# Kernel optimization log

Measured on AMD Instinct MI355X. Metric: run time of the kernel, lower is better.

Reference implementation:

```python
import jax, jax.numpy as jnp
import numpy as np
import math

D_MODEL = 1024
N_HEADS = 16
D_K = D_MODEL // N_HEADS
ROPE_BASE = 10000.0


def rope_cos_sin(seq_len, d_k, base=ROPE_BASE, dtype=jnp.float32):
    inv_freq = 1.0 / base ** (jnp.arange(0, d_k, 2, dtype=dtype) / d_k)  # [d_k/2]
    pos = jnp.arange(seq_len, dtype=dtype)
    freqs = jnp.outer(pos, inv_freq)  # [T, d_k/2]
    return jnp.cos(freqs), jnp.sin(freqs)


def apply_rope(x, cos, sin):
    # x: [B, H, T, d_k]; cos/sin: [T, d_k/2]
    x1 = x[..., 0::2]
    x2 = x[..., 1::2]
    c = cos[None, None]
    s = sin[None, None]
    r1 = x1 * c - x2 * s
    r2 = x1 * s + x2 * c
    return jnp.stack([r1, r2], axis=-1).reshape(x.shape)


def setup_inputs() -> dict:
    key = jax.random.key(0)
    ks = jax.random.split(key, 7)
    B, T = 2, 2048
    scale = 1.0 / math.sqrt(D_MODEL)
    return {
        "query": jax.random.normal(ks[0], (B, T, D_MODEL), jnp.float32),
        "key": jax.random.normal(ks[1], (B, T, D_MODEL), jnp.float32),
        "value": jax.random.normal(ks[2], (B, T, D_MODEL), jnp.float32),
        "Wq": jax.random.normal(ks[3], (D_MODEL, D_MODEL), jnp.float32) * scale,
        "Wk": jax.random.normal(ks[4], (D_MODEL, D_MODEL), jnp.float32) * scale,
        "Wv": jax.random.normal(ks[5], (D_MODEL, D_MODEL), jnp.float32) * scale,
        "Wo": jax.random.normal(ks[6], (D_MODEL, D_MODEL), jnp.float32) * scale,
    }


def reference(query, key, value, Wq, Wk, Wv, Wo):
    B, Tq, _ = query.shape
    Tk = key.shape[1]
    # nn.Linear: x @ W.T
    Q = (query @ Wq.T).reshape(B, Tq, N_HEADS, D_K).transpose(0, 2, 1, 3)
    K = (key @ Wk.T).reshape(B, Tk, N_HEADS, D_K).transpose(0, 2, 1, 3)
    V = (value @ Wv.T).reshape(B, Tk, N_HEADS, D_K).transpose(0, 2, 1, 3)
    cos_q, sin_q = rope_cos_sin(Tq, D_K)
    cos_k, sin_k = rope_cos_sin(Tk, D_K)
    Q = apply_rope(Q, cos_q, sin_q)
    K = apply_rope(K, cos_k, sin_k)
    scores = jnp.einsum("bhqd,bhkd->bhqk", Q, K) / math.sqrt(D_K)
    attn = jax.nn.softmax(scores, axis=-1)
    out = jnp.einsum("bhqk,bhkd->bhqd", attn, V)
    out = out.transpose(0, 2, 1, 3).reshape(B, Tq, D_MODEL)
    return out @ Wo.T
```

## Files before the change

kernel.cpp:

```cpp
#include <hip/hip_runtime.h>
#include <hip/hip_bf16.h>
#include <cstdint>

typedef unsigned short u16;
typedef __attribute__((ext_vector_type(4))) float fl4;
typedef __attribute__((ext_vector_type(2))) float fl2;
typedef __attribute__((ext_vector_type(4))) unsigned short u16x4;
typedef __attribute__((ext_vector_type(8))) unsigned short u16x8;
typedef __attribute__((ext_vector_type(2))) unsigned int u32x2;
typedef __attribute__((ext_vector_type(8))) __bf16 bf16x8;
typedef __attribute__((ext_vector_type(4))) float f32x4;

#define MKE 4194304
#define NKE 1048576

static __device__ __forceinline__ u16 f2bf(float x) {
  unsigned int u = __builtin_bit_cast(unsigned int, x);
  u += 0x7fffu + ((u >> 16) & 1u);
  return (u16)(u >> 16);
}

static __device__ __forceinline__ unsigned int cvtpk(float a, float b) {
  unsigned int r;
  asm("v_cvt_pk_bf16_f32 %0, %1, %2" : "=v"(r) : "v"(a), "v"(b));
  return r;
}

static __device__ __forceinline__ f32x4 mfma16(bf16x8 a, bf16x8 b, f32x4 c) {
  return __builtin_amdgcn_mfma_f32_16x16x32_bf16(a, b, c, 0, 0, 0);
}

static __device__ __forceinline__ void gload_lds16(const void* g, void* l) {
  __builtin_amdgcn_global_load_lds((const __attribute__((address_space(1))) void*)g,
                                   (__attribute__((address_space(3))) void*)l,
                                   16, 0, 0);
}

__global__ __launch_bounds__(256) void k_prep(const float* __restrict__ q,
                                              const float* __restrict__ k,
                                              const float* __restrict__ v,
                                              const float* __restrict__ wq,
                                              const float* __restrict__ wk,
                                              const float* __restrict__ wv,
                                              const float* __restrict__ wo,
                                              u16* __restrict__ ws,
                                              float* __restrict__ tab) {
  const int bid = blockIdx.x;
  if (bid >= 16384) {
    const int idx = (bid - 16384) * 256 + threadIdx.x;
    const int t = idx >> 5, i = idx & 31;
    const float ang = (float)t * exp2f(-0.4152410118609203f * (float)i);
    float sn, cs;
    sincosf(ang, &sn, &cs);
    reinterpret_cast<fl2*>(tab)[idx] = (fl2){cs, sn};
    return;
  }
  const int i = bid * 256 + threadIdx.x;
  const float* src;
  u16* dst;
  int loc;
  if (i < 3 * 1048576) {
    const int seg = i >> 20;
    loc = i & 1048575;
    src = seg == 0 ? q : (seg == 1 ? k : v);
    dst = ws + (size_t)seg * MKE;
  } else {
    const int j = i - 3 * 1048576;
    const int seg = j >> 18;
    loc = j & 262143;
    src = seg == 0 ? wq : (seg == 1 ? wk : (seg == 2 ? wv : wo));
    dst = ws + 3 * (size_t)MKE + (size_t)seg * NKE;
  }
  fl4 val = reinterpret_cast<const fl4*>(src)[loc];
  u16x4 o;
  o[0] = f2bf(val[0]); o[1] = f2bf(val[1]); o[2] = f2bf(val[2]); o[3] = f2bf(val[3]);
  reinterpret_cast<u16x4*>(dst)[loc] = o;
}

__global__ __launch_bounds__(256) void k_gemm_qkv(
    const u16* __restrict__ aq, const u16* __restrict__ ak, const u16* __restrict__ av,
    const u16* __restrict__ bq, const u16* __restrict__ bk, const u16* __restrict__ bv,
    u16* __restrict__ cq, u16* __restrict__ ck, u16* __restrict__ cv,
    const fl2* __restrict__ tab) {
  constexpr int K = 1024;
  __shared__ __align__(16) u16 smem[16384];
  u16* sA = smem;
  u16* sB = smem + 8192;
  const int z = blockIdx.z;
  const u16* A  = z == 0 ? aq : (z == 1 ? ak : av);
  const u16* Bw = z == 0 ? bq : (z == 1 ? bk : bv);
  u16* C        = z == 0 ? cq : (z == 1 ? ck : cv);
  const float scale = (z == 0) ? 0.18033688011112042f : 1.0f;

  const int tid = threadIdx.x;
  const int w = tid >> 6, lane = tid & 63;
  const int wm = w >> 1, wn = w & 1;
  const int trow = blockIdx.y << 7, tcol = blockIdx.x << 7;
  const int l15 = lane & 15, l4 = lane >> 4;
  const int srow = lane >> 3;
  const int scol = ((lane & 7) ^ srow) << 3;

  f32x4 acc[4][4];
#pragma unroll
  for (int m = 0; m < 4; ++m)
#pragma unroll
    for (int n = 0; n < 4; ++n) acc[m][n] = (f32x4){0.f, 0.f, 0.f, 0.f};

  for (int k0 = 0; k0 < K; k0 += 64) {
#pragma unroll
    for (int c = 0; c < 4; ++c) {
      const int g = c * 4 + w;
      const int row = g * 8 + srow;
      gload_lds16(A + (size_t)(trow + row) * K + (k0 + scol), (void*)(sA + g * 512));
      gload_lds16(Bw + (size_t)(tcol + row) * K + (k0 + scol), (void*)(sB + g * 512));
    }
    __syncthreads();
#pragma unroll
    for (int kc = 0; kc < 2; ++kc) {
      const int kb = (kc * 32 + l4 * 8) * 2;
      bf16x8 af[4], bfr[4];
#pragma unroll
      for (int m = 0; m < 4; ++m) {
        const int r = wm * 64 + m * 16 + l15;
        af[m] = *reinterpret_cast<const bf16x8*>(
            reinterpret_cast<const char*>(sA) + r * 128 + (kb ^ ((r & 7) << 4)));
      }
#pragma unroll
      for (int n = 0; n < 4; ++n) {
        const int r = wn * 64 + n * 16 + l15;
        bfr[n] = *reinterpret_cast<const bf16x8*>(
            reinterpret_cast<const char*>(sB) + r * 128 + (kb ^ ((r & 7) << 4)));
      }
      __builtin_amdgcn_s_setprio(1);
#pragma unroll
      for (int m = 0; m < 4; ++m)
#pragma unroll
        for (int n = 0; n < 4; ++n)
          acc[m][n] = mfma16(af[m], bfr[n], acc[m][n]);
      __builtin_amdgcn_s_setprio(0);
    }
    __syncthreads();
  }

  if (z < 2) {
#pragma unroll
    for (int m = 0; m < 4; ++m) {
#pragma unroll
      for (int n = 0; n < 4; ++n) {
#pragma unroll
        for (int r = 0; r < 4; ++r) {
          const float vsc = acc[m][n][r] * scale;
          const int row = trow + wm * 64 + m * 16 + l4 * 4 + r;
          const int col = tcol + wn * 64 + n * 16 + l15;
          const int b = row >> 11, t = row & 2047;
          const int h = col >> 6, d = col & 63;
          const float partner = __shfl_xor(vsc, 1);
          const fl2 cs = tab[t * 32 + (d >> 1)];
          const float outv =
              (d & 1) ? (partner * cs.y + vsc * cs.x) : (vsc * cs.x - partner * cs.y);
          C[((size_t)((b << 4) + h) * 2048 + t) * 64 + d] = f2bf(outv);
        }
      }
    }
  } else {
#pragma unroll
    for (int m = 0; m < 4; ++m)
#pragma unroll
      for (int n = 0; n < 4; ++n)
#pragma unroll
        for (int r = 0; r < 4; ++r) {
          const int c = wn * 64 + n * 16 + l15;
          const int rl = wm * 64 + m * 16 + l4 * 4 + r;
          smem[c * 128 + (rl ^ ((c & 15) * 8))] = f2bf(acc[m][n][r]);
        }
    __syncthreads();
    const int bq = trow >> 11;
    const int tb = trow & 2047;
#pragma unroll
    for (int j = 0; j < 8; ++j) {
      const int flat = (tid + j * 256) * 8;
      const int c = flat >> 7, r0 = flat & 127;
      u16x8 vv = *reinterpret_cast<const u16x8*>(smem + c * 128 + (r0 ^ ((c & 15) * 8)));
      const int col = tcol + c;
      u16* dst = C + ((size_t)((bq << 4) + (col >> 6)) * 64 + (col & 63)) * 2048 + tb + r0;
      *reinterpret_cast<u16x8*>(dst) = vv;
    }
  }
}

__global__ __launch_bounds__(256) void k_gemm_o(const u16* __restrict__ A,
                                                const u16* __restrict__ Bw,
                                                float* __restrict__ C) {
  constexpr int K = 1024, N = 1024;
  __shared__ __align__(16) u16 sA[2][128 * 64];
  __shared__ __align__(16) u16 sB[2][64 * 64];
  const int tid = threadIdx.x;
  const int w = tid >> 6, lane = tid & 63;
  const int wm = w >> 1, wn = w & 1;
  const int trow = blockIdx.y << 7, tcol = blockIdx.x << 6;
  const int l15 = lane & 15, l4 = lane >> 4;
  const int srow = lane >> 3;
  const int scol = ((lane & 7) ^ srow) << 3;

  f32x4 acc[4][2];
#pragma unroll
  for (int m = 0; m < 4; ++m)
#pragma unroll
    for (int n = 0; n < 2; ++n) acc[m][n] = (f32x4){0.f, 0.f, 0.f, 0.f};

  auto stage = [&](int k0, int buf) {
#pragma unroll
    for (int c = 0; c < 4; ++c) {
      const int g = c * 4 + w;
      const int row = g * 8 + srow;
      gload_lds16(A + (size_t)(trow + row) * K + (k0 + scol), (void*)(sA[buf] + g * 512));
    }
#pragma unroll
    for (int c = 0; c < 2; ++c) {
      const int g = c * 4 + w;
      const int row = g * 8 + srow;
      gload_lds16(Bw + (size_t)(tcol + row) * K + (k0 + scol), (void*)(sB[buf] + g * 512));
    }
  };

  stage(0, 0);
  __syncthreads();

  for (int t = 0; t < 16; ++t) {
    const int buf = t & 1;
    if (t + 1 < 16) stage((t + 1) * 64, buf ^ 1);
#pragma unroll
    for (int kc = 0; kc < 2; ++kc) {
      const int kb = (kc * 32 + l4 * 8) * 2;
      bf16x8 af[4], bfr[2];
#pragma unroll
      for (int m = 0; m < 4; ++m) {
        const int r = wm * 64 + m * 16 + l15;
        af[m] = *reinterpret_cast<const bf16x8*>(
            reinterpret_cast<const char*>(sA[buf]) + r * 128 + (kb ^ ((r & 7) << 4)));
      }
#pragma unroll
      for (int n = 0; n < 2; ++n) {
        const int r = wn * 32 + n * 16 + l15;
        bfr[n] = *reinterpret_cast<const bf16x8*>(
            reinterpret_cast<const char*>(sB[buf]) + r * 128 + (kb ^ ((r & 7) << 4)));
      }
      __builtin_amdgcn_s_setprio(1);
#pragma unroll
      for (int m = 0; m < 4; ++m)
#pragma unroll
        for (int n = 0; n < 2; ++n)
          acc[m][n] = mfma16(af[m], bfr[n], acc[m][n]);
      __builtin_amdgcn_s_setprio(0);
    }
    __syncthreads();
  }

#pragma unroll
  for (int m = 0; m < 4; ++m)
#pragma unroll
    for (int n = 0; n < 2; ++n)
#pragma unroll
      for (int r = 0; r < 4; ++r) {
        const int row = trow + wm * 64 + m * 16 + l4 * 4 + r;
        const int col = tcol + wn * 32 + n * 16 + l15;
        C[(size_t)row * N + col] = acc[m][n][r];
      }
}

__global__ __launch_bounds__(256) void k_attn(const u16* __restrict__ Q,
                                              const u16* __restrict__ Kh,
                                              const u16* __restrict__ Vt,
                                              u16* __restrict__ Oout) {
  __shared__ __align__(16) char lds[81920];
  const int tid = threadIdx.x;
  const int w = tid >> 6, lane = tid & 63;
  const int l15 = lane & 15, l4 = lane >> 4;
  const int nb = blockIdx.x;
  const int xcd = nb & 7, idx = nb >> 3;
  const int bh = xcd * 4 + (idx >> 4);
  const int q0 = (idx & 15) << 7;

  const u16* Qg = Q + (size_t)bh * (2048 * 64);
  const u16* Kg = Kh + (size_t)bh * (2048 * 64);
  const u16* Vg = Vt + (size_t)bh * (64 * 2048);

  const int swz = (l15 & 7) << 4;
  const int rk0 = l15 * 128 + ((l4 * 16) ^ swz);
  const int rk1 = rk0 ^ 64;
  const int pbase = 65536 + w * 4096 + l15 * 128;
  int pwvA[4];
#pragma unroll
  for (int nn = 0; nn < 4; ++nn) pwvA[nn] = pbase + (((nn * 32) | (l4 * 8)) ^ swz);
  const int rpA0 = pbase + ((l4 * 16) ^ swz);
  const int rpA1 = rpA0 ^ 64;
  const int wst = w * 1024;

  const int srow8 = lane >> 3;
  const int scol = ((lane & 7) ^ srow8) << 3;
  const u16* gK = Kg + (size_t)(w * 8 + srow8) * 64 + scol;
  const u16* gV = Vg + (size_t)(w * 8 + srow8) * 2048 + scol;

  bf16x8 qf0, qf1, qf2, qf3;
  {
    const u16* qpA = Qg + (size_t)(q0 + w * 32 + l15) * 64 + l4 * 8;
    qf0 = *reinterpret_cast<const bf16x8*>(qpA);
    qf1 = *reinterpret_cast<const bf16x8*>(qpA + 32);
    const u16* qpB = qpA + 16 * 64;
    qf2 = *reinterpret_cast<const bf16x8*>(qpB);
    qf3 = *reinterpret_cast<const bf16x8*>(qpB + 32);
  }

  f32x4 oA[4], oB[4];
#pragma unroll
  for (int nn = 0; nn < 4; ++nn) {
    oA[nn] = (f32x4){0.f, 0.f, 0.f, 0.f};
    oB[nn] = (f32x4){0.f, 0.f, 0.f, 0.f};
  }
  float lrunA = 0.f, lrunB = 0.f;

#define STAGE(BUF, STEP)                                                         \
  {                                                                              \
    const int ke = (STEP) * 8192;                                                \
    gload_lds16(gK + ke,        lds + (BUF) + wst);                              \
    gload_lds16(gK + ke + 2048, lds + (BUF) + wst + 4096);                       \
    gload_lds16(gK + ke + 4096, lds + (BUF) + wst + 8192);                       \
    gload_lds16(gK + ke + 6144, lds + (BUF) + wst + 12288);                      \
    const int ve = (STEP) * 128;                                                 \
    gload_lds16(gV + ve,             lds + 32768 + (BUF) + wst);                 \
    gload_lds16(gV + ve + 65536,     lds + 32768 + (BUF) + wst + 4096);          \
    gload_lds16(gV + ve + 64,        lds + 32768 + (BUF) + wst + 8192);          \
    gload_lds16(gV + ve + 65536 + 64, lds + 32768 + (BUF) + wst + 12288);        \
  }

#define ATTN_BODY(KOFF, VOFF)                                                    \
  {                                                                              \
    f32x4 sA[4], sB[4];                                                          \
    __builtin_amdgcn_s_setprio(1);                                               \
    _Pragma("unroll")                                                            \
    for (int nn = 0; nn < 4; ++nn) {                                             \
      bf16x8 kf = *(const bf16x8*)(lds + (KOFF) + rk0 + nn * 2048);              \
      sA[nn] = mfma16(kf, qf0, (f32x4){0.f, 0.f, 0.f, 0.f});                     \
      sB[nn] = mfma16(kf, qf2, (f32x4){0.f, 0.f, 0.f, 0.f});                     \
    }                                                                            \
    _Pragma("unroll")                                                            \
    for (int nn = 0; nn < 4; ++nn) {                                             \
      bf16x8 kf = *(const bf16x8*)(lds + (KOFF) + rk1 + nn * 2048);              \
      sA[nn] = mfma16(kf, qf1, sA[nn]);                                          \
      sB[nn] = mfma16(kf, qf3, sB[nn]);                                          \
    }                                                                            \
    __builtin_amdgcn_s_setprio(0);                                               \
    float ppA[4][4], ppB[4][4];                                                  \
    _Pragma("unroll")                                                            \
    for (int nn = 0; nn < 4; ++nn) {                                             \
      ppA[nn][0] = __builtin_amdgcn_exp2f(sA[nn][0]);                            \
      ppA[nn][1] = __builtin_amdgcn_exp2f(sA[nn][1]);                            \
      ppA[nn][2] = __builtin_amdgcn_exp2f(sA[nn][2]);                            \
      ppA[nn][3] = __builtin_amdgcn_exp2f(sA[nn][3]);                            \
      ppB[nn][0] = __builtin_amdgcn_exp2f(sB[nn][0]);                            \
      ppB[nn][1] = __builtin_amdgcn_exp2f(sB[nn][1]);                            \
      ppB[nn][2] = __builtin_amdgcn_exp2f(sB[nn][2]);                            \
      ppB[nn][3] = __builtin_amdgcn_exp2f(sB[nn][3]);                            \
    }                                                                            \
    _Pragma("unroll")                                                            \
    for (int nn = 0; nn < 4; ++nn) {                                             \
      u32x2 pkA, pkB;                                                            \
      pkA[0] = cvtpk(ppA[nn][0], ppA[nn][1]);                                    \
      pkA[1] = cvtpk(ppA[nn][2], ppA[nn][3]);                                    \
      pkB[0] = cvtpk(ppB[nn][0], ppB[nn][1]);                                    \
      pkB[1] = cvtpk(ppB[nn][2], ppB[nn][3]);                                    \
      *(u32x2*)(lds + pwvA[nn]) = pkA;                                           \
      *(u32x2*)(lds + pwvA[nn] + 2048) = pkB;                                    \
    }                                                                            \
    float rsA = ((ppA[0][0] + ppA[0][1]) + (ppA[0][2] + ppA[0][3])) +            \
                ((ppA[1][0] + ppA[1][1]) + (ppA[1][2] + ppA[1][3])) +            \
                ((ppA[2][0] + ppA[2][1]) + (ppA[2][2] + ppA[2][3])) +            \
                ((ppA[3][0] + ppA[3][1]) + (ppA[3][2] + ppA[3][3]));             \
    float rsB = ((ppB[0][0] + ppB[0][1]) + (ppB[0][2] + ppB[0][3])) +            \
                ((ppB[1][0] + ppB[1][1]) + (ppB[1][2] + ppB[1][3])) +            \
                ((ppB[2][0] + ppB[2][1]) + (ppB[2][2] + ppB[2][3])) +            \
                ((ppB[3][0] + ppB[3][1]) + (ppB[3][2] + ppB[3][3]));             \
    rsA += __shfl_xor(rsA, 16);                                                  \
    rsA += __shfl_xor(rsA, 32);                                                  \
    rsB += __shfl_xor(rsB, 16);                                                  \
    rsB += __shfl_xor(rsB, 32);                                                  \
    lrunA += rsA;                                                                \
    lrunB += rsB;                                                                \
    __builtin_amdgcn_s_setprio(1);                                               \
    _Pragma("unroll")                                                            \
    for (int kc = 0; kc < 2; ++kc) {                                             \
      const bf16x8 pfA = *(const bf16x8*)(lds + (kc ? rpA1 : rpA0));             \
      const bf16x8 pfB = *(const bf16x8*)(lds + (kc ? rpA1 : rpA0) + 2048);      \
      const int rkk = kc ? rk1 : rk0;                                            \
      _Pragma("unroll")                                                          \
      for (int nn = 0; nn < 4; ++nn) {                                           \
        bf16x8 vf = *(const bf16x8*)(lds + (VOFF) + rkk + nn * 2048);            \
        oA[nn] = mfma16(pfA, vf, oA[nn]);                                        \
        oB[nn] = mfma16(pfB, vf, oB[nn]);                                        \
      }                                                                          \
    }                                                                            \
    __builtin_amdgcn_s_setprio(0);                                               \
  }

  STAGE(0, 0)
  __syncthreads();

  int cur = 0;
  for (int c = 0; c < 16; ++c) {
    if (c < 15) STAGE(cur ^ 16384, c + 1)
    ATTN_BODY(cur, 32768 + cur)
    ATTN_BODY(cur + 8192, 32768 + cur + 8192)
    __syncthreads();
    cur ^= 16384;
  }
#undef ATTN_BODY
#undef STAGE

  const int b = bh >> 4, h = bh & 15;
  float lrA[4], lrB[4];
#pragma unroll
  for (int r = 0; r < 4; ++r) {
    const int src = (lane & 48) | (l4 * 4 + r);
    lrA[r] = 1.f / __shfl(lrunA, src);
    lrB[r] = 1.f / __shfl(lrunB, src);
  }
#pragma unroll
  for (int nn = 0; nn < 4; ++nn)
#pragma unroll
    for (int r = 0; r < 4; ++r) {
      const int tA = q0 + w * 32 + l4 * 4 + r;
      const int d = nn * 16 + l15;
      Oout[((size_t)(b * 2048 + tA)) * 1024 + h * 64 + d] = f2bf(oA[nn][r] * lrA[r]);
      Oout[((size_t)(b * 2048 + tA + 16)) * 1024 + h * 64 + d] = f2bf(oB[nn][r] * lrB[r]);
    }
}

extern "C" void kernel_launch(void* const* d_in, const int* in_sizes, int n_in,
                              void* d_out, int out_size, void* d_ws, size_t ws_size,
                              hipStream_t stream) {
  const float* q  = (const float*)d_in[0];
  const float* k  = (const float*)d_in[1];
  const float* v  = (const float*)d_in[2];
  const float* wq = (const float*)d_in[3];
  const float* wk = (const float*)d_in[4];
  const float* wv = (const float*)d_in[5];
  const float* wo = (const float*)d_in[6];

  u16* ws = (u16*)d_ws;
  u16* Xq  = ws;
  u16* Xk  = Xq + MKE;
  u16* Xv  = Xk + MKE;
  u16* Wqb = Xv + MKE;
  u16* Wkb = Wqb + NKE;
  u16* Wvb = Wkb + NKE;
  u16* Wob = Wvb + NKE;
  u16* Qr  = Wob + NKE;
  u16* Kr  = Qr + MKE;
  u16* Vtm = Kr + MKE;
  u16* Vtr = Vtm + MKE;
  u16* AO  = Vtr + MKE;
  float* tab = (float*)AO;

  k_prep<<<16640, 256, 0, stream>>>(q, k, v, wq, wk, wv, wo, ws, tab);
  k_gemm_qkv<<<dim3(8, 32, 3), 256, 0, stream>>>(Xq, Xk, Xv, Wqb, Wkb, Wvb,
                                                 Qr, Kr, Vtr, (const fl2*)tab);
  k_attn<<<512, 256, 0, stream>>>(Qr, Kr, Vtr, AO);
  k_gemm_o<<<dim3(16, 32), 256, 0, stream>>>(AO, Wob, (float*)d_out);
}
```

Baseline: 128.9 us.

## Switch attention kernel to 32x32x16 MFMA with transposed output accumulators

Rewrites the attention inner loop to use 32x32x16 bf16 MFMA tiles instead of 16x16x32, computing S with K as the A operand and accumulating O transposed so each lane owns one query row. This removes the cross-lane shuffles for row sums and the per-row normalizer broadcast, and reduces the instruction count per tile. It changes the P write layout in LDS and the output store pattern, which risks bank conflicts and less coalesced output writes.

New measurement: 136.1 us. 1.06x slower.

```diff
diff --git a/kernel.cpp b/kernel.cpp
--- a/kernel.cpp
+++ b/kernel.cpp
@@ -7,9 +7,9 @@
 typedef __attribute__((ext_vector_type(2))) float fl2;
 typedef __attribute__((ext_vector_type(4))) unsigned short u16x4;
 typedef __attribute__((ext_vector_type(8))) unsigned short u16x8;
-typedef __attribute__((ext_vector_type(2))) unsigned int u32x2;
 typedef __attribute__((ext_vector_type(8))) __bf16 bf16x8;
 typedef __attribute__((ext_vector_type(4))) float f32x4;
+typedef __attribute__((ext_vector_type(16))) float f32x16;
 
 #define MKE 4194304
 #define NKE 1048576
@@ -28,6 +28,10 @@
 
 static __device__ __forceinline__ f32x4 mfma16(bf16x8 a, bf16x8 b, f32x4 c) {
   return __builtin_amdgcn_mfma_f32_16x16x32_bf16(a, b, c, 0, 0, 0);
+}
+
+static __device__ __forceinline__ f32x16 mfma32(bf16x8 a, bf16x8 b, f32x16 c) {
+  return __builtin_amdgcn_mfma_f32_32x32x16_bf16(a, b, c, 0, 0, 0);
 }
 
 static __device__ __forceinline__ void gload_lds16(const void* g, void* l) {
@@ -275,7 +279,6 @@
   __shared__ __align__(16) char lds[81920];
   const int tid = threadIdx.x;
   const int w = tid >> 6, lane = tid & 63;
-  const int l15 = lane & 15, l4 = lane >> 4;
   const int nb = blockIdx.x;
   const int xcd = nb & 7, idx = nb >> 3;
   const int bh = xcd * 4 + (idx >> 4);
@@ -285,39 +288,30 @@
   const u16* Kg = Kh + (size_t)bh * (2048 * 64);
   const u16* Vg = Vt + (size_t)bh * (64 * 2048);
 
-  const int swz = (l15 & 7) << 4;
-  const int rk0 = l15 * 128 + ((l4 * 16) ^ swz);
-  const int rk1 = rk0 ^ 64;
-  const int pbase = 65536 + w * 4096 + l15 * 128;
-  int pwvA[4];
-#pragma unroll
-  for (int nn = 0; nn < 4; ++nn) pwvA[nn] = pbase + (((nn * 32) | (l4 * 8)) ^ swz);
-  const int rpA0 = pbase + ((l4 * 16) ^ swz);
-  const int rpA1 = rpA0 ^ 64;
-  const int wst = w * 1024;
+  const int l31 = lane & 31, h = lane >> 5;
+  const int swz = l31 & 7;
+  const int ka0 = l31 * 128 + ((h ^ swz) << 4);
+  const int ka1 = ka0 ^ 32, ka2 = ka0 ^ 64, ka3 = ka0 ^ 96;
+
+  const int pbase = 65536 + w * 4096 + l31 * 128;
+  const int pwb = pbase + 8 * h;
+  const int rp0 = pbase + ((h ^ swz) << 4);
 
   const int srow8 = lane >> 3;
   const int scol = ((lane & 7) ^ srow8) << 3;
   const u16* gK = Kg + (size_t)(w * 8 + srow8) * 64 + scol;
   const u16* gV = Vg + (size_t)(w * 8 + srow8) * 2048 + scol;
-
-  bf16x8 qf0, qf1, qf2, qf3;
+  const int wst = w * 1024;
+
+  bf16x8 qfr[4];
   {
-    const u16* qpA = Qg + (size_t)(q0 + w * 32 + l15) * 64 + l4 * 8;
-    qf0 = *reinterpret_cast<const bf16x8*>(qpA);
-    qf1 = *reinterpret_cast<const bf16x8*>(qpA + 32);
-    const u16* qpB = qpA + 16 * 64;
-    qf2 = *reinterpret_cast<const bf16x8*>(qpB);
-    qf3 = *reinterpret_cast<const bf16x8*>(qpB + 32);
-  }
-
-  f32x4 oA[4], oB[4];
-#pragma unroll
-  for (int nn = 0; nn < 4; ++nn) {
-    oA[nn] = (f32x4){0.f, 0.f, 0.f, 0.f};
-    oB[nn] = (f32x4){0.f, 0.f, 0.f, 0.f};
-  }
-  float lrunA = 0.f, lrunB = 0.f;
+    const u16* qp = Qg + (size_t)(q0 + w * 32 + l31) * 64 + h * 8;
+#pragma unroll
+    for (int dc = 0; dc < 4; ++dc) qfr[dc] = *reinterpret_cast<const bf16x8*>(qp + dc * 16);
+  }
+
+  f32x16 oT0 = (f32x16)(0.f), oT1 = (f32x16)(0.f);
+  float lrun = 0.f;
 
 #define STAGE(BUF, STEP)                                                         \
   {                                                                              \
@@ -327,77 +321,64 @@
     gload_lds16(gK + ke + 4096, lds + (BUF) + wst + 8192);                       \
     gload_lds16(gK + ke + 6144, lds + (BUF) + wst + 12288);                      \
     const int ve = (STEP) * 128;                                                 \
-    gload_lds16(gV + ve,             lds + 32768 + (BUF) + wst);                 \
-    gload_lds16(gV + ve + 65536,     lds + 32768 + (BUF) + wst + 4096);          \
-    gload_lds16(gV + ve + 64,        lds + 32768 + (BUF) + wst + 8192);          \
+    gload_lds16(gV + ve,              lds + 32768 + (BUF) + wst);                \
+    gload_lds16(gV + ve + 65536,      lds + 32768 + (BUF) + wst + 4096);         \
+    gload_lds16(gV + ve + 64,         lds + 32768 + (BUF) + wst + 8192);         \
     gload_lds16(gV + ve + 65536 + 64, lds + 32768 + (BUF) + wst + 12288);        \
   }
 
 #define ATTN_BODY(KOFF, VOFF)                                                    \
   {                                                                              \
-    f32x4 sA[4], sB[4];                                                          \
+    f32x16 s0, s1;                                                               \
     __builtin_amdgcn_s_setprio(1);                                               \
-    _Pragma("unroll")                                                            \
-    for (int nn = 0; nn < 4; ++nn) {                                             \
-      bf16x8 kf = *(const bf16x8*)(lds + (KOFF) + rk0 + nn * 2048);              \
-      sA[nn] = mfma16(kf, qf0, (f32x4){0.f, 0.f, 0.f, 0.f});                     \
-      sB[nn] = mfma16(kf, qf2, (f32x4){0.f, 0.f, 0.f, 0.f});                     \
-    }                                                                            \
-    _Pragma("unroll")                                                            \
-    for (int nn = 0; nn < 4; ++nn) {                                             \
-      bf16x8 kf = *(const bf16x8*)(lds + (KOFF) + rk1 + nn * 2048);              \
-      sA[nn] = mfma16(kf, qf1, sA[nn]);                                          \
-      sB[nn] = mfma16(kf, qf3, sB[nn]);                                          \
+    {                                                                            \
+      bf16x8 kf;                                                                 \
+      kf = *(const bf16x8*)(lds + (KOFF) + ka0);        s0 = mfma32(kf, qfr[0], (f32x16)(0.f)); \
+      kf = *(const bf16x8*)(lds + (KOFF) + ka1);        s0 = mfma32(kf, qfr[1], s0); \
+      kf = *(const bf16x8*)(lds + (KOFF) + ka2);        s0 = mfma32(kf, qfr[2], s0); \
+      kf = *(const bf16x8*)(lds + (KOFF) + ka3);        s0 = mfma32(kf, qfr[3], s0); \
+      kf = *(const bf16x8*)(lds + (KOFF) + 4096 + ka0); s1 = mfma32(kf, qfr[0], (f32x16)(0.f)); \
+      kf = *(const bf16x8*)(lds + (KOFF) + 4096 + ka1); s1 = mfma32(kf, qfr[1], s1); \
+      kf = *(const bf16x8*)(lds + (KOFF) + 4096 + ka2); s1 = mfma32(kf, qfr[2], s1); \
+      kf = *(const bf16x8*)(lds + (KOFF) + 4096 + ka3); s1 = mfma32(kf, qfr[3], s1); \
     }                                                                            \
     __builtin_amdgcn_s_setprio(0);                                               \
-    float ppA[4][4], ppB[4][4];                                                  \
-    _Pragma("unroll")                                                            \
-    for (int nn = 0; nn < 4; ++nn) {                                             \
-      ppA[nn][0] = __builtin_amdgcn_exp2f(sA[nn][0]);                            \
-      ppA[nn][1] = __builtin_amdgcn_exp2f(sA[nn][1]);                            \
-      ppA[nn][2] = __builtin_amdgcn_exp2f(sA[nn][2]);                            \
-      ppA[nn][3] = __builtin_amdgcn_exp2f(sA[nn][3]);                            \
-      ppB[nn][0] = __builtin_amdgcn_exp2f(sB[nn][0]);                            \
-      ppB[nn][1] = __builtin_amdgcn_exp2f(sB[nn][1]);                            \
-      ppB[nn][2] = __builtin_amdgcn_exp2f(sB[nn][2]);                            \
-      ppB[nn][3] = __builtin_amdgcn_exp2f(sB[nn][3]);                            \
+    float rs = 0.f;                                                              \
+    {                                                                            \
+      float p0[16], p1[16];                                                      \
+      _Pragma("unroll")                                                          \
+      for (int r = 0; r < 16; ++r) p0[r] = __builtin_amdgcn_exp2f(s0[r]);        \
+      _Pragma("unroll")                                                          \
+      for (int r = 0; r < 16; ++r) p1[r] = __builtin_amdgcn_exp2f(s1[r]);        \
+      _Pragma("unroll")                                                          \
+      for (int r = 0; r < 16; ++r) rs += p0[r] + p1[r];                          \
+       \
+       \
+      _Pragma("unroll")                                                          \
+      for (int m = 0; m < 8; ++m) {                                              \
+        *(unsigned int*)(lds + pwb + ((((m >> 1)) ^ swz) << 4) + 4 * (m & 1)) =  \
+            cvtpk(p0[2 * m], p0[2 * m + 1]);                                     \
+        *(unsigned int*)(lds + pwb + ((((m >> 1) + 4) ^ swz) << 4) + 4 * (m & 1)) = \
+            cvtpk(p1[2 * m], p1[2 * m + 1]);                                     \
+      }                                                                          \
     }                                                                            \
-    _Pragma("unroll")                                                            \
-    for (int nn = 0; nn < 4; ++nn) {                                             \
-      u32x2 pkA, pkB;                                                            \
-      pkA[0] = cvtpk(ppA[nn][0], ppA[nn][1]);                                    \
-      pkA[1] = cvtpk(ppA[nn][2], ppA[nn][3]);                                    \
-      pkB[0] = cvtpk(ppB[nn][0], ppB[nn][1]);                                    \
-      pkB[1] = cvtpk(ppB[nn][2], ppB[nn][3]);                                    \
-      *(u32x2*)(lds + pwvA[nn]) = pkA;                                           \
-      *(u32x2*)(lds + pwvA[nn] + 2048) = pkB;                                    \
-    }                                                                            \
-    float rsA = ((ppA[0][0] + ppA[0][1]) + (ppA[0][2] + ppA[0][3])) +            \
-                ((ppA[1][0] + ppA[1][1]) + (ppA[1][2] + ppA[1][3])) +            \
-                ((ppA[2][0] + ppA[2][1]) + (ppA[2][2] + ppA[2][3])) +            \
-                ((ppA[3][0] + ppA[3][1]) + (ppA[3][2] + ppA[3][3]));             \
-    float rsB = ((ppB[0][0] + ppB[0][1]) + (ppB[0][2] + ppB[0][3])) +            \
-                ((ppB[1][0] + ppB[1][1]) + (ppB[1][2] + ppB[1][3])) +            \
-                ((ppB[2][0] + ppB[2][1]) + (ppB[2][2] + ppB[2][3])) +            \
-                ((ppB[3][0] + ppB[3][1]) + (ppB[3][2] + ppB[3][3]));             \
-    rsA += __shfl_xor(rsA, 16);                                                  \
-    rsA += __shfl_xor(rsA, 32);                                                  \
-    rsB += __shfl_xor(rsB, 16);                                                  \
-    rsB += __shfl_xor(rsB, 32);                                                  \
-    lrunA += rsA;                                                                \
-    lrunB += rsB;                                                                \
+    rs += __shfl_xor(rs, 32);                                                    \
+    lrun += rs;                                                                  \
     __builtin_amdgcn_s_setprio(1);                                               \
-    _Pragma("unroll")                                                            \
-    for (int kc = 0; kc < 2; ++kc) {                                             \
-      const bf16x8 pfA = *(const bf16x8*)(lds + (kc ? rpA1 : rpA0));             \
-      const bf16x8 pfB = *(const bf16x8*)(lds + (kc ? rpA1 : rpA0) + 2048);      \
-      const int rkk = kc ? rk1 : rk0;                                            \
-      _Pragma("unroll")                                                          \
-      for (int nn = 0; nn < 4; ++nn) {                                           \
-        bf16x8 vf = *(const bf16x8*)(lds + (VOFF) + rkk + nn * 2048);            \
-        oA[nn] = mfma16(pfA, vf, oA[nn]);                                        \
-        oB[nn] = mfma16(pfB, vf, oB[nn]);                                        \
-      }                                                                          \
+    {                                                                            \
+      bf16x8 vf, pf;                                                             \
+      pf = *(const bf16x8*)(lds + (rp0 ^ 0));                                    \
+      vf = *(const bf16x8*)(lds + (VOFF) + ka0);        oT0 = mfma32(vf, pf, oT0); \
+      vf = *(const bf16x8*)(lds + (VOFF) + 4096 + ka0); oT1 = mfma32(vf, pf, oT1); \
+      pf = *(const bf16x8*)(lds + (rp0 ^ 32));                                   \
+      vf = *(const bf16x8*)(lds + (VOFF) + ka1);        oT0 = mfma32(vf, pf, oT0); \
+      vf = *(const bf16x8*)(lds + (VOFF) + 4096 + ka1); oT1 = mfma32(vf, pf, oT1); \
+      pf = *(const bf16x8*)(lds + (rp0 ^ 64));                                   \
+      vf = *(const bf16x8*)(lds + (VOFF) + ka2);        oT0 = mfma32(vf, pf, oT0); \
+      vf = *(const bf16x8*)(lds + (VOFF) + 4096 + ka2); oT1 = mfma32(vf, pf, oT1); \
+      pf = *(const bf16x8*)(lds + (rp0 ^ 96));                                   \
+      vf = *(const bf16x8*)(lds + (VOFF) + ka3);        oT0 = mfma32(vf, pf, oT0); \
+      vf = *(const bf16x8*)(lds + (VOFF) + 4096 + ka3); oT1 = mfma32(vf, pf, oT1); \
     }                                                                            \
     __builtin_amdgcn_s_setprio(0);                                               \
   }
@@ -416,23 +397,15 @@
 #undef ATTN_BODY
 #undef STAGE
 
-  const int b = bh >> 4, h = bh & 15;
-  float lrA[4], lrB[4];
-#pragma unroll
-  for (int r = 0; r < 4; ++r) {
-    const int src = (lane & 48) | (l4 * 4 + r);
-    lrA[r] = 1.f / __shfl(lrunA, src);
-    lrB[r] = 1.f / __shfl(lrunB, src);
-  }
-#pragma unroll
-  for (int nn = 0; nn < 4; ++nn)
-#pragma unroll
-    for (int r = 0; r < 4; ++r) {
-      const int tA = q0 + w * 32 + l4 * 4 + r;
-      const int d = nn * 16 + l15;
-      Oout[((size_t)(b * 2048 + tA)) * 1024 + h * 64 + d] = f2bf(oA[nn][r] * lrA[r]);
-      Oout[((size_t)(b * 2048 + tA + 16)) * 1024 + h * 64 + d] = f2bf(oB[nn][r] * lrB[r]);
-    }
+  const int bq = bh >> 4, hd = bh & 15;
+  const float inv = 1.f / lrun;
+  u16* ob = Oout + ((size_t)(bq * 2048 + q0 + w * 32 + l31)) * 1024 + hd * 64;
+#pragma unroll
+  for (int r = 0; r < 16; ++r) {
+    const int dr = (r & 3) + 8 * (r >> 2) + 4 * h;
+    ob[dr] = f2bf(oT0[r] * inv);
+    ob[32 + dr] = f2bf(oT1[r] * inv);
+  }
 }
 
 extern "C" void kernel_launch(void* const* d_in, const int* in_sizes, int n_in,
```

## Double-buffer QKV GEMM loads and shrink its N tile to 64

Applied to the files above, without the earlier changes.

The QKV projection GEMM now uses double-buffered LDS tiles: the next K-slice is issued before the current one is computed, so global-to-LDS loads overlap the MFMAs. The N tile drops from 128 to 64 columns, one head per block, which doubles the grid to 1536 blocks and simplifies the RoPE and V-transpose epilogue indexing. Occupancy rises and the tail is shorter, but each A tile is reused across fewer columns, so more A traffic and more per-block overhead.

Measured after the change: 127.1 us. Within noise of the previous version (-1.4%).

```diff
diff --git a/kernel.cpp b/kernel.cpp
--- a/kernel.cpp
+++ b/kernel.cpp
@@ -83,9 +83,8 @@
     u16* __restrict__ cq, u16* __restrict__ ck, u16* __restrict__ cv,
     const fl2* __restrict__ tab) {
   constexpr int K = 1024;
-  __shared__ __align__(16) u16 smem[16384];
-  u16* sA = smem;
-  u16* sB = smem + 8192;
+  __shared__ __align__(16) u16 sA[2][128 * 64];
+  __shared__ __align__(16) u16 sB[2][64 * 64];
   const int z = blockIdx.z;
   const u16* A  = z == 0 ? aq : (z == 1 ? ak : av);
   const u16* Bw = z == 0 ? bq : (z == 1 ? bk : bv);
@@ -95,65 +94,77 @@
   const int tid = threadIdx.x;
   const int w = tid >> 6, lane = tid & 63;
   const int wm = w >> 1, wn = w & 1;
-  const int trow = blockIdx.y << 7, tcol = blockIdx.x << 7;
+  const int trow = blockIdx.y << 7, tcol = blockIdx.x << 6;
   const int l15 = lane & 15, l4 = lane >> 4;
   const int srow = lane >> 3;
   const int scol = ((lane & 7) ^ srow) << 3;
 
-  f32x4 acc[4][4];
+  f32x4 acc[4][2];
 #pragma unroll
   for (int m = 0; m < 4; ++m)
 #pragma unroll
-    for (int n = 0; n < 4; ++n) acc[m][n] = (f32x4){0.f, 0.f, 0.f, 0.f};
-
-  for (int k0 = 0; k0 < K; k0 += 64) {
+    for (int n = 0; n < 2; ++n) acc[m][n] = (f32x4){0.f, 0.f, 0.f, 0.f};
+
+  auto stage = [&](int k0, int buf) {
 #pragma unroll
     for (int c = 0; c < 4; ++c) {
       const int g = c * 4 + w;
       const int row = g * 8 + srow;
-      gload_lds16(A + (size_t)(trow + row) * K + (k0 + scol), (void*)(sA + g * 512));
-      gload_lds16(Bw + (size_t)(tcol + row) * K + (k0 + scol), (void*)(sB + g * 512));
-    }
-    __syncthreads();
+      gload_lds16(A + (size_t)(trow + row) * K + (k0 + scol), (void*)(sA[buf] + g * 512));
+    }
+#pragma unroll
+    for (int c = 0; c < 2; ++c) {
+      const int g = c * 4 + w;
+      const int row = g * 8 + srow;
+      gload_lds16(Bw + (size_t)(tcol + row) * K + (k0 + scol), (void*)(sB[buf] + g * 512));
+    }
+  };
+
+  stage(0, 0);
+  __syncthreads();
+
+  for (int t = 0; t < 16; ++t) {
+    const int buf = t & 1;
+    if (t + 1 < 16) stage((t + 1) * 64, buf ^ 1);
 #pragma unroll
     for (int kc = 0; kc < 2; ++kc) {
       const int kb = (kc * 32 + l4 * 8) * 2;
-      bf16x8 af[4], bfr[4];
+      bf16x8 af[4], bfr[2];
 #pragma unroll
       for (int m = 0; m < 4; ++m) {
         const int r = wm * 64 + m * 16 + l15;
         af[m] = *reinterpret_cast<const bf16x8*>(
-            reinterpret_cast<const char*>(sA) + r * 128 + (kb ^ ((r & 7) << 4)));
-      }
-#pragma unroll
-      for (int n = 0; n < 4; ++n) {
-        const int r = wn * 64 + n * 16 + l15;
+            reinterpret_cast<const char*>(sA[buf]) + r * 128 + (kb ^ ((r & 7) << 4)));
+      }
+#pragma unroll
+      for (int n = 0; n < 2; ++n) {
+        const int r = wn * 32 + n * 16 + l15;
         bfr[n] = *reinterpret_cast<const bf16x8*>(
-            reinterpret_cast<const char*>(sB) + r * 128 + (kb ^ ((r & 7) << 4)));
+            reinterpret_cast<const char*>(sB[buf]) + r * 128 + (kb ^ ((r & 7) << 4)));
       }
       __builtin_amdgcn_s_setprio(1);
 #pragma unroll
       for (int m = 0; m < 4; ++m)
 #pragma unroll
-        for (int n = 0; n < 4; ++n)
+        for (int n = 0; n < 2; ++n)
           acc[m][n] = mfma16(af[m], bfr[n], acc[m][n]);
       __builtin_amdgcn_s_setprio(0);
     }
     __syncthreads();
   }
 
+  const int b = trow >> 11, tb = trow & 2047;
+  const int h = tcol >> 6;
   if (z < 2) {
 #pragma unroll
     for (int m = 0; m < 4; ++m) {
 #pragma unroll
-      for (int n = 0; n < 4; ++n) {
+      for (int n = 0; n < 2; ++n) {
 #pragma unroll
         for (int r = 0; r < 4; ++r) {
           const float vsc = acc[m][n][r] * scale;
-          const int row = trow + wm * 64 + m * 16 + l4 * 4 + r;
-          const int col = tcol + wn * 64 + n * 16 + l15;
-          const int b = row >> 11, t = row & 2047;
-          const int h = col >> 6, d = col & 63;
+          const int t = tb + wm * 64 + m * 16 + l4 * 4 + r;
+          const int d = wn * 32 + n * 16 + l15;
           const float partner = __shfl_xor(vsc, 1);
           const fl2 cs = tab[t * 32 + (d >> 1)];
           const float outv =
@@ -163,26 +174,24 @@
       }
     }
   } else {
+    u16* smem = sA[0];
 #pragma unroll
     for (int m = 0; m < 4; ++m)
 #pragma unroll
-      for (int n = 0; n < 4; ++n)
+      for (int n = 0; n < 2; ++n)
 #pragma unroll
         for (int r = 0; r < 4; ++r) {
-          const int c = wn * 64 + n * 16 + l15;
+          const int dl = wn * 32 + n * 16 + l15;
           const int rl = wm * 64 + m * 16 + l4 * 4 + r;
-          smem[c * 128 + (rl ^ ((c & 15) * 8))] = f2bf(acc[m][n][r]);
+          smem[dl * 128 + (rl ^ ((dl & 15) * 8))] = f2bf(acc[m][n][r]);
         }
     __syncthreads();
-    const int bq = trow >> 11;
-    const int tb = trow & 2047;
-#pragma unroll
-    for (int j = 0; j < 8; ++j) {
+#pragma unroll
+    for (int j = 0; j < 4; ++j) {
       const int flat = (tid + j * 256) * 8;
-      const int c = flat >> 7, r0 = flat & 127;
-      u16x8 vv = *reinterpret_cast<const u16x8*>(smem + c * 128 + (r0 ^ ((c & 15) * 8)));
-      const int col = tcol + c;
-      u16* dst = C + ((size_t)((bq << 4) + (col >> 6)) * 64 + (col & 63)) * 2048 + tb + r0;
+      const int dl = flat >> 7, t0 = flat & 127;
+      u16x8 vv = *reinterpret_cast<const u16x8*>(smem + dl * 128 + (t0 ^ ((dl & 15) * 8)));
+      u16* dst = C + ((size_t)((b << 4) + h) * 64 + dl) * 2048 + tb + t0;
       *reinterpret_cast<u16x8*>(dst) = vv;
     }
   }
@@ -327,9 +336,9 @@
     gload_lds16(gK + ke + 4096, lds + (BUF) + wst + 8192);                       \
     gload_lds16(gK + ke + 6144, lds + (BUF) + wst + 12288);                      \
     const int ve = (STEP) * 128;                                                 \
-    gload_lds16(gV + ve,             lds + 32768 + (BUF) + wst);                 \
-    gload_lds16(gV + ve + 65536,     lds + 32768 + (BUF) + wst + 4096);          \
-    gload_lds16(gV + ve + 64,        lds + 32768 + (BUF) + wst + 8192);          \
+    gload_lds16(gV + ve,              lds + 32768 + (BUF) + wst);                \
+    gload_lds16(gV + ve + 65536,      lds + 32768 + (BUF) + wst + 4096);         \
+    gload_lds16(gV + ve + 64,         lds + 32768 + (BUF) + wst + 8192);         \
     gload_lds16(gV + ve + 65536 + 64, lds + 32768 + (BUF) + wst + 12288);        \
   }
 
@@ -462,8 +471,8 @@
   float* tab = (float*)AO;
 
   k_prep<<<16640, 256, 0, stream>>>(q, k, v, wq, wk, wv, wo, ws, tab);
-  k_gemm_qkv<<<dim3(8, 32, 3), 256, 0, stream>>>(Xq, Xk, Xv, Wqb, Wkb, Wvb,
-                                                 Qr, Kr, Vtr, (const fl2*)tab);
+  k_gemm_qkv<<<dim3(16, 32, 3), 256, 0, stream>>>(Xq, Xk, Xv, Wqb, Wkb, Wvb,
+                                                  Qr, Kr, Vtr, (const fl2*)tab);
   k_attn<<<512, 256, 0, stream>>>(Qr, Kr, Vtr, AO);
   k_gemm_o<<<dim3(16, 32), 256, 0, stream>>>(AO, Wob, (float*)d_out);
 }
```
